# Performance work log

Hardware: AMD Instinct MI355X
Metric: run time of the kernel (lower is better)

The kernel has to match this reference:

```python
import jax, jax.numpy as jnp
import numpy as np

N_NODES = 50000
N_EDGES = 800000
IN_DIM = 128
HID = 64
HEADS = 4
OUT_DIM = 128
NEG_SLOPE = 0.2


def setup_inputs() -> dict:
    key = jax.random.key(0)
    ks = jax.random.split(key, 11)
    x = jax.random.normal(ks[0], (N_NODES, IN_DIM), dtype=jnp.float32)
    edge_index = jax.random.randint(ks[1], (2, N_EDGES), 0, N_NODES, dtype=jnp.int64)
    s1 = 1.0 / np.sqrt(IN_DIM)
    s2 = 1.0 / np.sqrt(HEADS * HID)
    W1 = jax.random.normal(ks[2], (IN_DIM, HEADS * HID), dtype=jnp.float32) * s1
    a_src1 = jax.random.normal(ks[3], (HEADS, HID), dtype=jnp.float32) * s2
    a_dst1 = jax.random.normal(ks[4], (HEADS, HID), dtype=jnp.float32) * s2
    b1 = jnp.zeros((HEADS * HID,), dtype=jnp.float32)
    W2 = jax.random.normal(ks[5], (HEADS * HID, OUT_DIM), dtype=jnp.float32) * s2
    a_src2 = jax.random.normal(ks[6], (1, OUT_DIM), dtype=jnp.float32) * 0.1
    a_dst2 = jax.random.normal(ks[7], (1, OUT_DIM), dtype=jnp.float32) * 0.1
    b2 = jnp.zeros((OUT_DIM,), dtype=jnp.float32)
    return {"x": x, "edge_index": edge_index, "W1": W1, "a_src1": a_src1,
            "a_dst1": a_dst1, "b1": b1, "W2": W2, "a_src2": a_src2,
            "a_dst2": a_dst2, "b2": b2}


def _gat_conv(x, src, dst, W, a_src, a_dst, bias, heads, out_per_head, concat):
    n = x.shape[0]
    # linear projection per head: [N, H, F]
    h = (x @ W).reshape(n, heads, out_per_head)
    # per-node attention terms: [N, H]
    alpha_src = jnp.einsum('nhf,hf->nh', h, a_src)
    alpha_dst = jnp.einsum('nhf,hf->nh', h, a_dst)
    # edge logits with LeakyReLU: [E, H]
    e = jax.nn.leaky_relu(alpha_src[src] + alpha_dst[dst], NEG_SLOPE)
    # softmax over incoming edges of each destination node
    m = jax.ops.segment_max(e, dst, num_segments=n)  # [N, H]
    m = jnp.where(jnp.isfinite(m), m, 0.0)
    e = jnp.exp(e - m[dst])
    denom = jax.ops.segment_sum(e, dst, num_segments=n)  # [N, H]
    alpha = e / (denom[dst] + 1e-16)  # [E, H]
    # weighted scatter-aggregate of source messages
    out = jax.ops.segment_sum(h[src] * alpha[:, :, None], dst, num_segments=n)  # [N, H, F]
    if concat:
        out = out.reshape(n, heads * out_per_head)
    else:
        out = out.mean(axis=1)
    return out + bias


def reference(x, edge_index, W1, a_src1, a_dst1, b1, W2, a_src2, a_dst2, b2):
    n = x.shape[0]
    # PyG GATConv adds self-loops by default
    loops = jnp.arange(n, dtype=edge_index.dtype)
    src = jnp.concatenate([edge_index[0], loops])
    dst = jnp.concatenate([edge_index[1], loops])
    # dropout layers are identity in inference
    h = _gat_conv(x, src, dst, W1, a_src1, a_dst1, b1, HEADS, HID, True)
    h = jax.nn.elu(h)
    out = _gat_conv(h, src, dst, W2, a_src2, a_dst2, b2, 1, OUT_DIM, True)
    # F.normalize(p=2, dim=1)
    norm = jnp.linalg.norm(out, axis=1, keepdims=True)
    return out / jnp.maximum(norm, 1e-12)
```

## Files before the change

kernel.cpp:

```cpp
#include <hip/hip_runtime.h>
#include <hip/hip_fp16.h>
#include <math.h>

#define N_NODES 50000
#define N_EDGES 800000
#define ET (N_EDGES + N_NODES)
#define IN_DIM 128
#define HID 64
#define HEADS 4
#define C1 (HEADS * HID)
#define OUT_DIM 128
#define NEG_SLOPE 0.2f
#define MTILES 3125
#define SCAN_B 1024
#define NSCB 49

typedef _Float16 h8 __attribute__((ext_vector_type(8)));
typedef float f4 __attribute__((ext_vector_type(4)));

__device__ __forceinline__ float leaky(float v) { return fmaxf(v, NEG_SLOPE * v); }
__device__ __forceinline__ float elu(float v) { return v > 0.0f ? v : expm1f(v); }

__device__ __forceinline__ void fma_mix8(float* acc, h8 v, float w) {
    union { h8 h; int i[4]; } u; u.h = v;
#pragma unroll
    for (int k = 0; k < 4; ++k) {
        asm("v_fma_mix_f32 %0, %1, %2, %0 op_sel:[0,0,0] op_sel_hi:[1,0,0]"
            : "+v"(acc[2 * k]) : "v"(u.i[k]), "v"(w));
        asm("v_fma_mix_f32 %0, %1, %2, %0 op_sel:[1,0,0] op_sel_hi:[1,0,0]"
            : "+v"(acc[2 * k + 1]) : "v"(u.i[k]), "v"(w));
    }
}

__global__ void prep_kernel(const float* __restrict__ W1, const float* __restrict__ W2,
                            const int* __restrict__ dst, __half* __restrict__ w1t,
                            __half* __restrict__ w2t, int* __restrict__ cnt) {
    const int tid = blockIdx.x * blockDim.x + threadIdx.x;
    const int np = gridDim.x * blockDim.x;
    for (int i = tid; i < IN_DIM * C1; i += np) {
        int k1 = i >> 8, n1 = i & 255;
        w1t[n1 * IN_DIM + k1] = __float2half(W1[i]);
        int k2 = i >> 7, n2 = i & 127;
        w2t[n2 * C1 + k2] = __float2half(W2[i]);
    }
    for (int i = tid; i < ET; i += np) {
        int d = (i < N_EDGES) ? dst[i] : i - N_EDGES;
        atomicAdd(&cnt[d], 1);
    }
}

__global__ void scan_local(const int* __restrict__ cnt, int* __restrict__ lscan,
                           int* __restrict__ bsum) {
    __shared__ int wsum[16];
    const int t = threadIdx.x, lane = t & 63, wv = t >> 6;
    int idx = blockIdx.x * SCAN_B + t;
    int v = (idx < N_NODES) ? cnt[idx] : 0;
    int sc = v;
#pragma unroll
    for (int o = 1; o < 64; o <<= 1) {
        int u = __shfl_up(sc, o);
        if (lane >= o) sc += u;
    }
    if (lane == 63) wsum[wv] = sc;
    __syncthreads();
    if (t == 0) {
        int run = 0;
#pragma unroll
        for (int w = 0; w < 16; ++w) { int s = wsum[w]; wsum[w] = run; run += s; }
        bsum[blockIdx.x] = run;
    }
    __syncthreads();
    if (idx < N_NODES) lscan[idx] = sc + wsum[wv];
}

__global__ void scan_bsum(int* __restrict__ bsum) {
    const int t = threadIdx.x;
    int v = (t < NSCB) ? bsum[t] : 0;
    int sc = v;
#pragma unroll
    for (int o = 1; o < 64; o <<= 1) {
        int u = __shfl_up(sc, o);
        if (t >= o) sc += u;
    }
    if (t < NSCB) bsum[t] = sc - v;
}

__global__ void scan_final(const int* __restrict__ cnt, const int* __restrict__ lscan,
                           const int* __restrict__ bsum, int* __restrict__ rp,
                           int* __restrict__ cursor) {
    int idx = blockIdx.x * SCAN_B + threadIdx.x;
    if (idx == 0) rp[0] = 0;
    if (idx >= N_NODES) return;
    int inc = lscan[idx] + bsum[idx >> 10];
    rp[idx + 1] = inc;
    cursor[idx] = inc - cnt[idx];
}

__global__ void scatter_kernel(const int* __restrict__ src, const int* __restrict__ dst,
                               int* __restrict__ cursor, int* __restrict__ col_src) {
    int i = blockIdx.x * blockDim.x + threadIdx.x;
    if (i >= ET) return;
    int s, d;
    if (i < N_EDGES) { s = src[i]; d = dst[i]; } else { s = d = i - N_EDGES; }
    int pos = atomicAdd(&cursor[d], 1);
    col_src[pos] = s;
}

__global__ __launch_bounds__(256) void gemm1_mfma(
        const float* __restrict__ x, const __half* __restrict__ w1t,
        const float* __restrict__ aws, const float* __restrict__ awd,
        __half* __restrict__ hpm, float* __restrict__ as1m, float* __restrict__ ad1m) {
    const int tile = blockIdx.x * 4 + (threadIdx.x >> 6);
    if (tile >= MTILES) return;
    const int lane = threadIdx.x & 63;
    const int m0 = tile * 16, lm = lane & 15, lq = lane >> 4;
    h8 afrag[4];
    const float4* xrow = (const float4*)(x + (size_t)(m0 + lm) * IN_DIM + lq * 8);
#pragma unroll
    for (int kt = 0; kt < 4; ++kt) {
        float4 a = xrow[kt * 8];
        float4 b = xrow[kt * 8 + 1];
        union { h8 v; __half2 p[4]; } u;
        u.p[0] = __floats2half2_rn(a.x, a.y);
        u.p[1] = __floats2half2_rn(a.z, a.w);
        u.p[2] = __floats2half2_rn(b.x, b.y);
        u.p[3] = __floats2half2_rn(b.z, b.w);
        afrag[kt] = u.v;
    }
    f4 acc[16];
#pragma unroll
    for (int nt = 0; nt < 16; ++nt) acc[nt] = (f4){0.f, 0.f, 0.f, 0.f};
#pragma unroll
    for (int nt = 0; nt < 16; ++nt) {
        const h8* brow = (const h8*)(w1t + (size_t)(nt * 16 + lm) * IN_DIM + lq * 8);
#pragma unroll
        for (int kt = 0; kt < 4; ++kt)
            acc[nt] = __builtin_amdgcn_mfma_f32_16x16x32_f16(afrag[kt], brow[kt * 4],
                                                             acc[nt], 0, 0, 0);
    }
    float sS[4][4] = {{0.f}}, sD[4][4] = {{0.f}};
#pragma unroll
    for (int nt = 0; nt < 16; ++nt) {
        int col = nt * 16 + lm;
        float wa = aws[col], wd = awd[col];
        int hd = nt >> 2;
        int pr = nt >> 3;
        int cip = col & 127;
#pragma unroll
        for (int r = 0; r < 4; ++r) {
            float v = acc[nt][r];
            hpm[((size_t)pr * N_NODES + (m0 + lq * 4 + r)) * 128 + cip] = __float2half(v);
            sS[hd][r] += v * wa;
            sD[hd][r] += v * wd;
        }
    }
#pragma unroll
    for (int o = 1; o < 16; o <<= 1) {
#pragma unroll
        for (int hd = 0; hd < 4; ++hd)
#pragma unroll
            for (int r = 0; r < 4; ++r) {
                sS[hd][r] += __shfl_xor(sS[hd][r], o);
                sD[hd][r] += __shfl_xor(sD[hd][r], o);
            }
    }
    if (lm == 0) {
        float2* asp = (float2*)as1m;
        float2* adp = (float2*)ad1m;
#pragma unroll
        for (int r = 0; r < 4; ++r) {
            int row = m0 + lq * 4 + r;
            asp[row]           = make_float2(sS[0][r], sS[1][r]);
            asp[N_NODES + row] = make_float2(sS[2][r], sS[3][r]);
            adp[row]           = make_float2(sD[0][r], sD[1][r]);
            adp[N_NODES + row] = make_float2(sD[2][r], sD[3][r]);
        }
    }
}

__global__ __launch_bounds__(256) void gemm2_mfma(
        const __half* __restrict__ ah, const __half* __restrict__ w2t,
        const float* __restrict__ aws, const float* __restrict__ awd,
        __half* __restrict__ h, float* __restrict__ as2, float* __restrict__ ad2) {
    const int tile = blockIdx.x * 4 + (threadIdx.x >> 6);
    if (tile >= MTILES) return;
    const int lane = threadIdx.x & 63;
    const int m0 = tile * 16, lm = lane & 15, lq = lane >> 4;
    h8 afrag[8];
    const h8* arow = (const h8*)(ah + (size_t)(m0 + lm) * C1 + lq * 8);
#pragma unroll
    for (int kt = 0; kt < 8; ++kt) afrag[kt] = arow[kt * 4];
    f4 acc[8];
#pragma unroll
    for (int nt = 0; nt < 8; ++nt) acc[nt] = (f4){0.f, 0.f, 0.f, 0.f};
#pragma unroll
    for (int nt = 0; nt < 8; ++nt) {
        const h8* brow = (const h8*)(w2t + (size_t)(nt * 16 + lm) * C1 + lq * 8);
#pragma unroll
        for (int kt = 0; kt < 8; ++kt)
            acc[nt] = __builtin_amdgcn_mfma_f32_16x16x32_f16(afrag[kt], brow[kt * 4],
                                                             acc[nt], 0, 0, 0);
    }
    float sS[4] = {0.f, 0.f, 0.f, 0.f}, sD[4] = {0.f, 0.f, 0.f, 0.f};
#pragma unroll
    for (int nt = 0; nt < 8; ++nt) {
        int col = nt * 16 + lm;
        float wa = aws[col], wd = awd[col];
#pragma unroll
        for (int r = 0; r < 4; ++r) {
            float v = acc[nt][r];
            h[(size_t)(m0 + lq * 4 + r) * OUT_DIM + col] = __float2half(v);
            sS[r] += v * wa;
            sD[r] += v * wd;
        }
    }
#pragma unroll
    for (int o = 1; o < 16; o <<= 1) {
#pragma unroll
        for (int r = 0; r < 4; ++r) {
            sS[r] += __shfl_xor(sS[r], o);
            sD[r] += __shfl_xor(sD[r], o);
        }
    }
    if (lm == 0) {
#pragma unroll
        for (int r = 0; r < 4; ++r) {
            int row = m0 + lq * 4 + r;
            as2[row] = sS[r];
            ad2[row] = sD[r];
        }
    }
}

__global__ __launch_bounds__(256) void aggregate1_fused(
        const int* __restrict__ rp, const int* __restrict__ cs,
        const __half* __restrict__ hpm, const float* __restrict__ as1m,
        const float* __restrict__ ad1m, const float* __restrict__ b1,
        __half* __restrict__ out1h) {
    __shared__ int4 stg[8][32];
    const int pair = blockIdx.x & 1, g = blockIdx.x >> 1;
    const int hw = threadIdx.x >> 5, li = threadIdx.x & 31;
    const int d = g * 8 + hw;
    const int e0 = rp[d], deg = rp[d + 1] - e0;
    const float2* asb = (const float2*)as1m + (size_t)pair * N_NODES;
    const float2 adv = ((const float2*)ad1m)[(size_t)pair * N_NODES + d];
    const char* hb = (const char*)hpm + (size_t)pair * N_NODES * 256;
    const int es = li >> 4, fl = li & 15;
    const int hip = fl >> 3;
    const int lbyte = fl * 16;
    float acc[8] = {0.f, 0.f, 0.f, 0.f, 0.f, 0.f, 0.f, 0.f};
    float ds0 = 0.f, ds1 = 0.f;
    for (int c0 = 0; c0 < deg; c0 += 32) {
        const int clen = min(32, deg - c0);
        int idx = c0 + li;
        bool valid = idx < deg;
        int s = valid ? cs[e0 + idx] : 0;
        float2 av = asb[s];
        float x0 = valid ? __expf(leaky(av.x + adv.x)) : 0.f;
        float x1 = valid ? __expf(leaky(av.y + adv.y)) : 0.f;
        stg[hw][li] = make_int4(s << 8, __float_as_int(x0), __float_as_int(x1), 0);
        ds0 += x0; ds1 += x1;
        __builtin_amdgcn_wave_barrier();
        int j = 0;
        for (; j + 8 <= clen; j += 8) {
            int4 p0 = stg[hw][j + es];
            int4 p1 = stg[hw][j + 2 + es];
            int4 p2 = stg[hw][j + 4 + es];
            int4 p3 = stg[hw][j + 6 + es];
            h8 v0 = *(const h8*)(hb + p0.x + lbyte);
            h8 v1 = *(const h8*)(hb + p1.x + lbyte);
            h8 v2 = *(const h8*)(hb + p2.x + lbyte);
            h8 v3 = *(const h8*)(hb + p3.x + lbyte);
            fma_mix8(acc, v0, __int_as_float(hip ? p0.z : p0.y));
            fma_mix8(acc, v1, __int_as_float(hip ? p1.z : p1.y));
            fma_mix8(acc, v2, __int_as_float(hip ? p2.z : p2.y));
            fma_mix8(acc, v3, __int_as_float(hip ? p3.z : p3.y));
        }
        for (; j < clen; j += 2) {
            int4 p0 = stg[hw][j + es];
            h8 v0 = *(const h8*)(hb + p0.x + lbyte);
            fma_mix8(acc, v0, __int_as_float(hip ? p0.z : p0.y));
        }
        __builtin_amdgcn_wave_barrier();
    }
#pragma unroll
    for (int f = 0; f < 8; ++f) acc[f] += __shfl_xor(acc[f], 16);
#pragma unroll
    for (int o = 16; o > 0; o >>= 1) {
        ds0 += __shfl_xor(ds0, o);
        ds1 += __shfl_xor(ds1, o);
    }
    if (es == 0) {
        float den = hip ? ds1 : ds0;
        float inv = 1.0f / (den + 1e-16f);
        float4 bA = ((const float4*)b1)[pair * 32 + fl * 2];
        float4 bB = ((const float4*)b1)[pair * 32 + fl * 2 + 1];
        h8 o;
        o[0] = (_Float16)elu(acc[0] * inv + bA.x);
        o[1] = (_Float16)elu(acc[1] * inv + bA.y);
        o[2] = (_Float16)elu(acc[2] * inv + bA.z);
        o[3] = (_Float16)elu(acc[3] * inv + bA.w);
        o[4] = (_Float16)elu(acc[4] * inv + bB.x);
        o[5] = (_Float16)elu(acc[5] * inv + bB.y);
        o[6] = (_Float16)elu(acc[6] * inv + bB.z);
        o[7] = (_Float16)elu(acc[7] * inv + bB.w);
        *(h8*)((char*)out1h + (size_t)d * 512 + pair * 256 + lbyte) = o;
    }
}

__global__ __launch_bounds__(256) void aggregate2_fused(
        const int* __restrict__ rp, const int* __restrict__ cs,
        const __half* __restrict__ h2h, const float* __restrict__ as2,
        const float* __restrict__ ad2, const float* __restrict__ b2,
        float* __restrict__ out) {
    __shared__ int2 stg[8][32];
    const int hw = threadIdx.x >> 5, li = threadIdx.x & 31;
    const int d = blockIdx.x * 8 + hw;
    const int e0 = rp[d], deg = rp[d + 1] - e0;
    const float adv = ad2[d];
    const int q = li >> 4, lo = li & 15;
    const int lbyte = lo * 16;
    const char* hbase = (const char*)h2h;
    float acc[8] = {0.f, 0.f, 0.f, 0.f, 0.f, 0.f, 0.f, 0.f};
    float dsum = 0.f;
    for (int c0 = 0; c0 < deg; c0 += 32) {
        const int clen = min(32, deg - c0);
        int idx = c0 + li;
        bool valid = idx < deg;
        int s = valid ? cs[e0 + idx] : 0;
        float x = valid ? __expf(leaky(as2[s] + adv)) : 0.f;
        stg[hw][li] = make_int2(valid ? (s << 8) : 0, __float_as_int(x));
        dsum += x;
        __builtin_amdgcn_wave_barrier();
        int j = 0;
        for (; j + 8 <= clen; j += 8) {
            int2 p0 = stg[hw][j + q];
            int2 p1 = stg[hw][j + 2 + q];
            int2 p2 = stg[hw][j + 4 + q];
            int2 p3 = stg[hw][j + 6 + q];
            h8 v0 = *(const h8*)(hbase + p0.x + lbyte);
            h8 v1 = *(const h8*)(hbase + p1.x + lbyte);
            h8 v2 = *(const h8*)(hbase + p2.x + lbyte);
            h8 v3 = *(const h8*)(hbase + p3.x + lbyte);
            fma_mix8(acc, v0, __int_as_float(p0.y));
            fma_mix8(acc, v1, __int_as_float(p1.y));
            fma_mix8(acc, v2, __int_as_float(p2.y));
            fma_mix8(acc, v3, __int_as_float(p3.y));
        }
        for (; j < clen; j += 2) {
            int2 p0 = stg[hw][j + q];
            h8 v0 = *(const h8*)(hbase + p0.x + lbyte);
            fma_mix8(acc, v0, __int_as_float(p0.y));
        }
        __builtin_amdgcn_wave_barrier();
    }
#pragma unroll
    for (int f = 0; f < 8; ++f) acc[f] += __shfl_xor(acc[f], 16);
#pragma unroll
    for (int o = 16; o > 0; o >>= 1) dsum += __shfl_xor(dsum, o);
    if (q == 0) {
        float inv = 1.0f / (dsum + 1e-16f);
        float4 bA = ((const float4*)b2)[lo * 2];
        float4 bB = ((const float4*)b2)[lo * 2 + 1];
        float v0 = acc[0] * inv + bA.x, v1 = acc[1] * inv + bA.y;
        float v2 = acc[2] * inv + bA.z, v3 = acc[3] * inv + bA.w;
        float v4 = acc[4] * inv + bB.x, v5 = acc[5] * inv + bB.y;
        float v6 = acc[6] * inv + bB.z, v7 = acc[7] * inv + bB.w;
        float ss = v0 * v0 + v1 * v1 + v2 * v2 + v3 * v3 +
                   v4 * v4 + v5 * v5 + v6 * v6 + v7 * v7;
#pragma unroll
        for (int o = 1; o < 16; o <<= 1) ss += __shfl_xor(ss, o);
        float sc = 1.0f / fmaxf(sqrtf(ss), 1e-12f);
        float4* orow = (float4*)((char*)out + (size_t)d * 512 + lo * 32);
        orow[0] = make_float4(v0 * sc, v1 * sc, v2 * sc, v3 * sc);
        orow[1] = make_float4(v4 * sc, v5 * sc, v6 * sc, v7 * sc);
    }
}

extern "C" void kernel_launch(void* const* d_in, const int* in_sizes, int n_in,
                              void* d_out, int out_size, void* d_ws, size_t ws_size,
                              hipStream_t stream) {
    const float* x     = (const float*)d_in[0];
    const int*   edge  = (const int*)d_in[1];
    const int*   src   = edge;
    const int*   dst   = edge + N_EDGES;
    const float* W1    = (const float*)d_in[2];
    const float* aw_s1 = (const float*)d_in[3];
    const float* aw_d1 = (const float*)d_in[4];
    const float* b1    = (const float*)d_in[5];
    const float* W2    = (const float*)d_in[6];
    const float* aw_s2 = (const float*)d_in[7];
    const float* aw_d2 = (const float*)d_in[8];
    const float* b2    = (const float*)d_in[9];
    float* out = (float*)d_out;

    char* ws = (char*)d_ws;
    size_t off = 0;
    auto alloc = [&](size_t bytes) {
        void* p = ws + off;
        off += (bytes + 255) & ~(size_t)255;
        return p;
    };
    int*    col_src = (int*)alloc((size_t)ET * 4);
    int*    rp     = (int*)alloc((size_t)(N_NODES + 1) * 4);
    int*    cursor = (int*)alloc((size_t)N_NODES * 4);
    int*    cnt    = (int*)alloc((size_t)N_NODES * 4);
    int*    lscan  = (int*)alloc((size_t)NSCB * SCAN_B * 4);
    int*    bsum   = (int*)alloc((size_t)NSCB * 4);
    float*  as1    = (float*)alloc((size_t)N_NODES * HEADS * 4);
    float*  ad1    = (float*)alloc((size_t)N_NODES * HEADS * 4);
    float*  as2    = (float*)alloc((size_t)N_NODES * 4);
    float*  ad2    = (float*)alloc((size_t)N_NODES * 4);
    __half* w1t    = (__half*)alloc((size_t)IN_DIM * C1 * 2);
    __half* w2t    = (__half*)alloc((size_t)C1 * OUT_DIM * 2);
    __half* hpm    = (__half*)alloc((size_t)N_NODES * C1 * 2);
    __half* out1h  = (__half*)alloc((size_t)N_NODES * C1 * 2);
    __half* h2h    = hpm;
    (void)off;

    hipMemsetAsync(cnt, 0, (size_t)N_NODES * 4, stream);

    const int egrid = (ET + 255) / 256;

    prep_kernel<<<1024, 256, 0, stream>>>(W1, W2, dst, w1t, w2t, cnt);
    scan_local<<<NSCB, SCAN_B, 0, stream>>>(cnt, lscan, bsum);
    scan_bsum<<<1, 64, 0, stream>>>(bsum);
    scan_final<<<NSCB, SCAN_B, 0, stream>>>(cnt, lscan, bsum, rp, cursor);
    scatter_kernel<<<egrid, 256, 0, stream>>>(src, dst, cursor, col_src);

    gemm1_mfma<<<(MTILES + 3) / 4, 256, 0, stream>>>(x, w1t, aw_s1, aw_d1, hpm, as1, ad1);
    aggregate1_fused<<<(N_NODES / 8) * 2, 256, 0, stream>>>(rp, col_src, hpm, as1, ad1, b1, out1h);

    gemm2_mfma<<<(MTILES + 3) / 4, 256, 0, stream>>>(out1h, w2t, aw_s2, aw_d2, h2h, as2, ad2);
    aggregate2_fused<<<N_NODES / 8, 256, 0, stream>>>(rp, col_src, h2h, as2, ad2, b2, out);
}
```

Measured before the change: 349.0 us.

## Split layer-2 features into column halves for aggregation, normalize in separate pass

gemm2 now writes its fp16 output in a column-split layout: two contiguous 64-column planes, each 128 bytes per node. aggregate2 runs twice as many blocks, and each block gathers only one half-plane, which matches how layer 1 is aggregated. The aim is a smaller gather footprint per block and more parallelism. Because each block now sees only half a row, the L2 norm is built by atomically adding partial sums into a new zeroed buffer. A separate norm_kernel then rescales the output, adding a launch and an extra read-write pass over the output.

```diff
diff --git a/kernel.cpp b/kernel.cpp
--- a/kernel.cpp
+++ b/kernel.cpp
@@ -181,7 +181,7 @@
 __global__ __launch_bounds__(256) void gemm2_mfma(
         const __half* __restrict__ ah, const __half* __restrict__ w2t,
         const float* __restrict__ aws, const float* __restrict__ awd,
-        __half* __restrict__ h, float* __restrict__ as2, float* __restrict__ ad2) {
+        __half* __restrict__ h2c, float* __restrict__ as2, float* __restrict__ ad2) {
     const int tile = blockIdx.x * 4 + (threadIdx.x >> 6);
     if (tile >= MTILES) return;
     const int lane = threadIdx.x & 63;
@@ -206,10 +206,12 @@
     for (int nt = 0; nt < 8; ++nt) {
         int col = nt * 16 + lm;
         float wa = aws[col], wd = awd[col];
+        int half = nt >> 2;
+        int cih = col & 63;
 #pragma unroll
         for (int r = 0; r < 4; ++r) {
             float v = acc[nt][r];
-            h[(size_t)(m0 + lq * 4 + r) * OUT_DIM + col] = __float2half(v);
+            h2c[((size_t)half * N_NODES + (m0 + lq * 4 + r)) * 64 + cih] = __float2half(v);
             sS[r] += v * wa;
             sD[r] += v * wd;
         }
@@ -308,19 +310,20 @@
     }
 }
 
-__global__ __launch_bounds__(256) void aggregate2_fused(
+__global__ __launch_bounds__(256) void aggregate2_half(
         const int* __restrict__ rp, const int* __restrict__ cs,
-        const __half* __restrict__ h2h, const float* __restrict__ as2,
+        const __half* __restrict__ h2c, const float* __restrict__ as2,
         const float* __restrict__ ad2, const float* __restrict__ b2,
-        float* __restrict__ out) {
+        float* __restrict__ out, float* __restrict__ ss) {
     __shared__ int2 stg[8][32];
+    const int half = blockIdx.x & 1, g = blockIdx.x >> 1;
     const int hw = threadIdx.x >> 5, li = threadIdx.x & 31;
-    const int d = blockIdx.x * 8 + hw;
+    const int d = g * 8 + hw;
     const int e0 = rp[d], deg = rp[d + 1] - e0;
     const float adv = ad2[d];
-    const int q = li >> 4, lo = li & 15;
-    const int lbyte = lo * 16;
-    const char* hbase = (const char*)h2h;
+    const char* hb = (const char*)h2c + (size_t)half * N_NODES * 128;
+    const int es = li >> 3, fl = li & 7;
+    const int lbyte = fl * 16;
     float acc[8] = {0.f, 0.f, 0.f, 0.f, 0.f, 0.f, 0.f, 0.f};
     float dsum = 0.f;
     for (int c0 = 0; c0 < deg; c0 += 32) {
@@ -328,53 +331,67 @@
         int idx = c0 + li;
         bool valid = idx < deg;
         int s = valid ? cs[e0 + idx] : 0;
-        float x = valid ? __expf(leaky(as2[s] + adv)) : 0.f;
-        stg[hw][li] = make_int2(valid ? (s << 8) : 0, __float_as_int(x));
-        dsum += x;
+        float xv = valid ? __expf(leaky(as2[s] + adv)) : 0.f;
+        stg[hw][li] = make_int2(s << 7, __float_as_int(xv));
+        dsum += xv;
         __builtin_amdgcn_wave_barrier();
         int j = 0;
-        for (; j + 8 <= clen; j += 8) {
-            int2 p0 = stg[hw][j + q];
-            int2 p1 = stg[hw][j + 2 + q];
-            int2 p2 = stg[hw][j + 4 + q];
-            int2 p3 = stg[hw][j + 6 + q];
-            h8 v0 = *(const h8*)(hbase + p0.x + lbyte);
-            h8 v1 = *(const h8*)(hbase + p1.x + lbyte);
-            h8 v2 = *(const h8*)(hbase + p2.x + lbyte);
-            h8 v3 = *(const h8*)(hbase + p3.x + lbyte);
+        for (; j + 16 <= clen; j += 16) {
+            int2 p0 = stg[hw][j + es];
+            int2 p1 = stg[hw][j + 4 + es];
+            int2 p2 = stg[hw][j + 8 + es];
+            int2 p3 = stg[hw][j + 12 + es];
+            h8 v0 = *(const h8*)(hb + p0.x + lbyte);
+            h8 v1 = *(const h8*)(hb + p1.x + lbyte);
+            h8 v2 = *(const h8*)(hb + p2.x + lbyte);
+            h8 v3 = *(const h8*)(hb + p3.x + lbyte);
             fma_mix8(acc, v0, __int_as_float(p0.y));
             fma_mix8(acc, v1, __int_as_float(p1.y));
             fma_mix8(acc, v2, __int_as_float(p2.y));
             fma_mix8(acc, v3, __int_as_float(p3.y));
         }
-        for (; j < clen; j += 2) {
-            int2 p0 = stg[hw][j + q];
-            h8 v0 = *(const h8*)(hbase + p0.x + lbyte);
+        for (; j < clen; j += 4) {
+            int2 p0 = stg[hw][j + es];
+            h8 v0 = *(const h8*)(hb + p0.x + lbyte);
             fma_mix8(acc, v0, __int_as_float(p0.y));
         }
         __builtin_amdgcn_wave_barrier();
     }
 #pragma unroll
-    for (int f = 0; f < 8; ++f) acc[f] += __shfl_xor(acc[f], 16);
+    for (int f = 0; f < 8; ++f) {
+        acc[f] += __shfl_xor(acc[f], 8);
+        acc[f] += __shfl_xor(acc[f], 16);
+    }
 #pragma unroll
     for (int o = 16; o > 0; o >>= 1) dsum += __shfl_xor(dsum, o);
-    if (q == 0) {
+    if (es == 0) {
         float inv = 1.0f / (dsum + 1e-16f);
-        float4 bA = ((const float4*)b2)[lo * 2];
-        float4 bB = ((const float4*)b2)[lo * 2 + 1];
+        float4 bA = ((const float4*)b2)[half * 16 + fl * 2];
+        float4 bB = ((const float4*)b2)[half * 16 + fl * 2 + 1];
         float v0 = acc[0] * inv + bA.x, v1 = acc[1] * inv + bA.y;
         float v2 = acc[2] * inv + bA.z, v3 = acc[3] * inv + bA.w;
         float v4 = acc[4] * inv + bB.x, v5 = acc[5] * inv + bB.y;
         float v6 = acc[6] * inv + bB.z, v7 = acc[7] * inv + bB.w;
-        float ss = v0 * v0 + v1 * v1 + v2 * v2 + v3 * v3 +
+        float sp = v0 * v0 + v1 * v1 + v2 * v2 + v3 * v3 +
                    v4 * v4 + v5 * v5 + v6 * v6 + v7 * v7;
 #pragma unroll
-        for (int o = 1; o < 16; o <<= 1) ss += __shfl_xor(ss, o);
-        float sc = 1.0f / fmaxf(sqrtf(ss), 1e-12f);
-        float4* orow = (float4*)((char*)out + (size_t)d * 512 + lo * 32);
-        orow[0] = make_float4(v0 * sc, v1 * sc, v2 * sc, v3 * sc);
-        orow[1] = make_float4(v4 * sc, v5 * sc, v6 * sc, v7 * sc);
-    }
+        for (int o = 1; o < 8; o <<= 1) sp += __shfl_xor(sp, o);
+        if (fl == 0) atomicAdd(&ss[d], sp);
+        float4* orow = (float4*)(out + (size_t)d * OUT_DIM + half * 64 + fl * 8);
+        orow[0] = make_float4(v0, v1, v2, v3);
+        orow[1] = make_float4(v4, v5, v6, v7);
+    }
+}
+
+__global__ __launch_bounds__(256) void norm_kernel(const float* __restrict__ ss,
+                                                   float* __restrict__ out) {
+    int idx = blockIdx.x * 256 + threadIdx.x;
+    int row = idx >> 5, c = idx & 31;
+    if (row >= N_NODES) return;
+    float sc = 1.0f / fmaxf(sqrtf(ss[row]), 1e-12f);
+    float4* p = (float4*)out + (size_t)row * 32 + c;
+    float4 v = *p;
+    *p = make_float4(v.x * sc, v.y * sc, v.z * sc, v.w * sc);
 }
 
 extern "C" void kernel_launch(void* const* d_in, const int* in_sizes, int n_in,
@@ -405,6 +422,7 @@
     int*    rp     = (int*)alloc((size_t)(N_NODES + 1) * 4);
     int*    cursor = (int*)alloc((size_t)N_NODES * 4);
     int*    cnt    = (int*)alloc((size_t)N_NODES * 4);
+    float*  ss     = (float*)alloc((size_t)N_NODES * 4);
     int*    lscan  = (int*)alloc((size_t)NSCB * SCAN_B * 4);
     int*    bsum   = (int*)alloc((size_t)NSCB * 4);
     float*  as1    = (float*)alloc((size_t)N_NODES * HEADS * 4);
@@ -415,10 +433,11 @@
     __half* w2t    = (__half*)alloc((size_t)C1 * OUT_DIM * 2);
     __half* hpm    = (__half*)alloc((size_t)N_NODES * C1 * 2);
     __half* out1h  = (__half*)alloc((size_t)N_NODES * C1 * 2);
-    __half* h2h    = hpm;
+    __half* h2c    = hpm;
     (void)off;
 
-    hipMemsetAsync(cnt, 0, (size_t)N_NODES * 4, stream);
+    const size_t cnt_rounded = ((size_t)N_NODES * 4 + 255) & ~(size_t)255;
+    hipMemsetAsync(cnt, 0, cnt_rounded + (size_t)N_NODES * 4, stream);
 
     const int egrid = (ET + 255) / 256;
 
@@ -431,6 +450,7 @@
     gemm1_mfma<<<(MTILES + 3) / 4, 256, 0, stream>>>(x, w1t, aw_s1, aw_d1, hpm, as1, ad1);
     aggregate1_fused<<<(N_NODES / 8) * 2, 256, 0, stream>>>(rp, col_src, hpm, as1, ad1, b1, out1h);
 
-    gemm2_mfma<<<(MTILES + 3) / 4, 256, 0, stream>>>(out1h, w2t, aw_s2, aw_d2, h2h, as2, ad2);
-    aggregate2_fused<<<N_NODES / 8, 256, 0, stream>>>(rp, col_src, h2h, as2, ad2, b2, out);
-}
+    gemm2_mfma<<<(MTILES + 3) / 4, 256, 0, stream>>>(out1h, w2t, aw_s2, aw_d2, h2c, as2, ad2);
+    aggregate2_half<<<(N_NODES / 8) * 2, 256, 0, stream>>>(rp, col_src, h2c, as2, ad2, b2, out, ss);
+    norm_kernel<<<(N_NODES * 32 + 255) / 256, 256, 0, stream>>>(ss, out);
+}
```

Result: slower. 364.0 us (+4.3%).

## Fuse edge scatter into gemm1 and store CSR source indices as 16-bit

Applied to the files above, without the earlier changes.

Merges the edge scatter kernel into the first GEMM launch by interleaving block roles: one in five blocks does an MFMA tile, the other four do scatter. This removes a kernel launch and lets the atomic scatter overlap with GEMM work. Column source indices are stored as uint16 to halve CSR index traffic, which depends on node ids staying below 65536. Both aggregation kernels also gain a 16-edge unrolled loop to keep more gathers in flight, at the cost of more register pressure.

```diff
diff --git a/kernel.cpp b/kernel.cpp
--- a/kernel.cpp
+++ b/kernel.cpp
@@ -14,9 +14,12 @@
 #define MTILES 3125
 #define SCAN_B 1024
 #define NSCB 49
+#define SCB 3328
+#define FUSED_GRID 4160
 
 typedef _Float16 h8 __attribute__((ext_vector_type(8)));
 typedef float f4 __attribute__((ext_vector_type(4)));
+typedef unsigned short u16;
 
 __device__ __forceinline__ float leaky(float v) { return fmaxf(v, NEG_SLOPE * v); }
 __device__ __forceinline__ float elu(float v) { return v > 0.0f ? v : expm1f(v); }
@@ -96,21 +99,25 @@
     cursor[idx] = inc - cnt[idx];
 }
 
-__global__ void scatter_kernel(const int* __restrict__ src, const int* __restrict__ dst,
-                               int* __restrict__ cursor, int* __restrict__ col_src) {
-    int i = blockIdx.x * blockDim.x + threadIdx.x;
-    if (i >= ET) return;
-    int s, d;
-    if (i < N_EDGES) { s = src[i]; d = dst[i]; } else { s = d = i - N_EDGES; }
-    int pos = atomicAdd(&cursor[d], 1);
-    col_src[pos] = s;
-}
-
-__global__ __launch_bounds__(256) void gemm1_mfma(
+__global__ __launch_bounds__(256) void gemm1_scatter(
         const float* __restrict__ x, const __half* __restrict__ w1t,
         const float* __restrict__ aws, const float* __restrict__ awd,
-        __half* __restrict__ hpm, float* __restrict__ as1m, float* __restrict__ ad1m) {
-    const int tile = blockIdx.x * 4 + (threadIdx.x >> 6);
+        __half* __restrict__ hpm, float* __restrict__ as1m, float* __restrict__ ad1m,
+        const int* __restrict__ src, const int* __restrict__ dst,
+        int* __restrict__ cursor, u16* __restrict__ cs16) {
+    const int q5 = blockIdx.x / 5, r5 = blockIdx.x % 5;
+    if (r5 != 0) {
+        int si = q5 * 4 + (r5 - 1);
+        int i = si * 256 + threadIdx.x;
+        if (i < ET) {
+            int s, d;
+            if (i < N_EDGES) { s = src[i]; d = dst[i]; } else { s = d = i - N_EDGES; }
+            int pos = atomicAdd(&cursor[d], 1);
+            cs16[pos] = (u16)s;
+        }
+        return;
+    }
+    const int tile = q5 * 4 + (threadIdx.x >> 6);
     if (tile >= MTILES) return;
     const int lane = threadIdx.x & 63;
     const int m0 = tile * 16, lm = lane & 15, lq = lane >> 4;
@@ -233,7 +240,7 @@
 }
 
 __global__ __launch_bounds__(256) void aggregate1_fused(
-        const int* __restrict__ rp, const int* __restrict__ cs,
+        const int* __restrict__ rp, const u16* __restrict__ cs16,
         const __half* __restrict__ hpm, const float* __restrict__ as1m,
         const float* __restrict__ ad1m, const float* __restrict__ b1,
         __half* __restrict__ out1h) {
@@ -254,7 +261,7 @@
         const int clen = min(32, deg - c0);
         int idx = c0 + li;
         bool valid = idx < deg;
-        int s = valid ? cs[e0 + idx] : 0;
+        int s = valid ? (int)cs16[e0 + idx] : 0;
         float2 av = asb[s];
         float x0 = valid ? __expf(leaky(av.x + adv.x)) : 0.f;
         float x1 = valid ? __expf(leaky(av.y + adv.y)) : 0.f;
@@ -262,6 +269,32 @@
         ds0 += x0; ds1 += x1;
         __builtin_amdgcn_wave_barrier();
         int j = 0;
+        for (; j + 16 <= clen; j += 16) {
+            int4 p0 = stg[hw][j + es];
+            int4 p1 = stg[hw][j + 2 + es];
+            int4 p2 = stg[hw][j + 4 + es];
+            int4 p3 = stg[hw][j + 6 + es];
+            int4 p4 = stg[hw][j + 8 + es];
+            int4 p5 = stg[hw][j + 10 + es];
+            int4 p6 = stg[hw][j + 12 + es];
+            int4 p7 = stg[hw][j + 14 + es];
+            h8 v0 = *(const h8*)(hb + p0.x + lbyte);
+            h8 v1 = *(const h8*)(hb + p1.x + lbyte);
+            h8 v2 = *(const h8*)(hb + p2.x + lbyte);
+            h8 v3 = *(const h8*)(hb + p3.x + lbyte);
+            h8 v4 = *(const h8*)(hb + p4.x + lbyte);
+            h8 v5 = *(const h8*)(hb + p5.x + lbyte);
+            h8 v6 = *(const h8*)(hb + p6.x + lbyte);
+            h8 v7 = *(const h8*)(hb + p7.x + lbyte);
+            fma_mix8(acc, v0, __int_as_float(hip ? p0.z : p0.y));
+            fma_mix8(acc, v1, __int_as_float(hip ? p1.z : p1.y));
+            fma_mix8(acc, v2, __int_as_float(hip ? p2.z : p2.y));
+            fma_mix8(acc, v3, __int_as_float(hip ? p3.z : p3.y));
+            fma_mix8(acc, v4, __int_as_float(hip ? p4.z : p4.y));
+            fma_mix8(acc, v5, __int_as_float(hip ? p5.z : p5.y));
+            fma_mix8(acc, v6, __int_as_float(hip ? p6.z : p6.y));
+            fma_mix8(acc, v7, __int_as_float(hip ? p7.z : p7.y));
+        }
         for (; j + 8 <= clen; j += 8) {
             int4 p0 = stg[hw][j + es];
             int4 p1 = stg[hw][j + 2 + es];
@@ -309,7 +342,7 @@
 }
 
 __global__ __launch_bounds__(256) void aggregate2_fused(
-        const int* __restrict__ rp, const int* __restrict__ cs,
+        const int* __restrict__ rp, const u16* __restrict__ cs16,
         const __half* __restrict__ h2h, const float* __restrict__ as2,
         const float* __restrict__ ad2, const float* __restrict__ b2,
         float* __restrict__ out) {
@@ -327,12 +360,38 @@
         const int clen = min(32, deg - c0);
         int idx = c0 + li;
         bool valid = idx < deg;
-        int s = valid ? cs[e0 + idx] : 0;
-        float x = valid ? __expf(leaky(as2[s] + adv)) : 0.f;
-        stg[hw][li] = make_int2(valid ? (s << 8) : 0, __float_as_int(x));
-        dsum += x;
+        int s = valid ? (int)cs16[e0 + idx] : 0;
+        float xv = valid ? __expf(leaky(as2[s] + adv)) : 0.f;
+        stg[hw][li] = make_int2(s << 8, __float_as_int(xv));
+        dsum += xv;
         __builtin_amdgcn_wave_barrier();
         int j = 0;
+        for (; j + 16 <= clen; j += 16) {
+            int2 p0 = stg[hw][j + q];
+            int2 p1 = stg[hw][j + 2 + q];
+            int2 p2 = stg[hw][j + 4 + q];
+            int2 p3 = stg[hw][j + 6 + q];
+            int2 p4 = stg[hw][j + 8 + q];
+            int2 p5 = stg[hw][j + 10 + q];
+            int2 p6 = stg[hw][j + 12 + q];
+            int2 p7 = stg[hw][j + 14 + q];
+            h8 v0 = *(const h8*)(hbase + p0.x + lbyte);
+            h8 v1 = *(const h8*)(hbase + p1.x + lbyte);
+            h8 v2 = *(const h8*)(hbase + p2.x + lbyte);
+            h8 v3 = *(const h8*)(hbase + p3.x + lbyte);
+            h8 v4 = *(const h8*)(hbase + p4.x + lbyte);
+            h8 v5 = *(const h8*)(hbase + p5.x + lbyte);
+            h8 v6 = *(const h8*)(hbase + p6.x + lbyte);
+            h8 v7 = *(const h8*)(hbase + p7.x + lbyte);
+            fma_mix8(acc, v0, __int_as_float(p0.y));
+            fma_mix8(acc, v1, __int_as_float(p1.y));
+            fma_mix8(acc, v2, __int_as_float(p2.y));
+            fma_mix8(acc, v3, __int_as_float(p3.y));
+            fma_mix8(acc, v4, __int_as_float(p4.y));
+            fma_mix8(acc, v5, __int_as_float(p5.y));
+            fma_mix8(acc, v6, __int_as_float(p6.y));
+            fma_mix8(acc, v7, __int_as_float(p7.y));
+        }
         for (; j + 8 <= clen; j += 8) {
             int2 p0 = stg[hw][j + q];
             int2 p1 = stg[hw][j + 2 + q];
@@ -401,7 +460,7 @@
         off += (bytes + 255) & ~(size_t)255;
         return p;
     };
-    int*    col_src = (int*)alloc((size_t)ET * 4);
+    u16*    cs16   = (u16*)alloc((size_t)ET * 2);
     int*    rp     = (int*)alloc((size_t)(N_NODES + 1) * 4);
     int*    cursor = (int*)alloc((size_t)N_NODES * 4);
     int*    cnt    = (int*)alloc((size_t)N_NODES * 4);
@@ -420,17 +479,16 @@
 
     hipMemsetAsync(cnt, 0, (size_t)N_NODES * 4, stream);
 
-    const int egrid = (ET + 255) / 256;
-
     prep_kernel<<<1024, 256, 0, stream>>>(W1, W2, dst, w1t, w2t, cnt);
     scan_local<<<NSCB, SCAN_B, 0, stream>>>(cnt, lscan, bsum);
     scan_bsum<<<1, 64, 0, stream>>>(bsum);
     scan_final<<<NSCB, SCAN_B, 0, stream>>>(cnt, lscan, bsum, rp, cursor);
-    scatter_kernel<<<egrid, 256, 0, stream>>>(src, dst, cursor, col_src);
-
-    gemm1_mfma<<<(MTILES + 3) / 4, 256, 0, stream>>>(x, w1t, aw_s1, aw_d1, hpm, as1, ad1);
-    aggregate1_fused<<<(N_NODES / 8) * 2, 256, 0, stream>>>(rp, col_src, hpm, as1, ad1, b1, out1h);
+
+    gemm1_scatter<<<FUSED_GRID, 256, 0, stream>>>(x, w1t, aw_s1, aw_d1, hpm, as1, ad1,
+                                                  src, dst, cursor, cs16);
+
+    aggregate1_fused<<<(N_NODES / 8) * 2, 256, 0, stream>>>(rp, cs16, hpm, as1, ad1, b1, out1h);
 
     gemm2_mfma<<<(MTILES + 3) / 4, 256, 0, stream>>>(out1h, w2t, aw_s2, aw_d2, h2h, as2, ad2);
-    aggregate2_fused<<<N_NODES / 8, 256, 0, stream>>>(rp, col_src, h2h, as2, ad2, b2, out);
-}
+    aggregate2_fused<<<N_NODES / 8, 256, 0, stream>>>(rp, cs16, h2h, as2, ad2, b2, out);
+}
```

New measurement: 332.1 us. 1.05x faster.

## Record atomic ranks during counting and store CSR columns as 16-bit

Applied to the files above, without the earlier changes.

The degree-counting pass now saves each edge's atomic return value as a 16-bit rank, so the scatter pass computes final CSR positions without a second round of atomics and the cursor array goes away. Self-loops are appended analytically at the end of each row instead of being counted. Column indices are stored as uint16, which halves index traffic in both aggregation kernels. This relies on N_NODES < 65536 and per-node degree fitting in 16 bits, and it changes the within-row order of edges.

```diff
diff --git a/kernel.cpp b/kernel.cpp
--- a/kernel.cpp
+++ b/kernel.cpp
@@ -17,6 +17,7 @@
 
 typedef _Float16 h8 __attribute__((ext_vector_type(8)));
 typedef float f4 __attribute__((ext_vector_type(4)));
+typedef unsigned short u16;
 
 __device__ __forceinline__ float leaky(float v) { return fmaxf(v, NEG_SLOPE * v); }
 __device__ __forceinline__ float elu(float v) { return v > 0.0f ? v : expm1f(v); }
@@ -34,7 +35,8 @@
 
 __global__ void prep_kernel(const float* __restrict__ W1, const float* __restrict__ W2,
                             const int* __restrict__ dst, __half* __restrict__ w1t,
-                            __half* __restrict__ w2t, int* __restrict__ cnt) {
+                            __half* __restrict__ w2t, int* __restrict__ cnt,
+                            u16* __restrict__ rank16) {
     const int tid = blockIdx.x * blockDim.x + threadIdx.x;
     const int np = gridDim.x * blockDim.x;
     for (int i = tid; i < IN_DIM * C1; i += np) {
@@ -43,9 +45,13 @@
         int k2 = i >> 7, n2 = i & 127;
         w2t[n2 * C1 + k2] = __float2half(W2[i]);
     }
-    for (int i = tid; i < ET; i += np) {
-        int d = (i < N_EDGES) ? dst[i] : i - N_EDGES;
-        atomicAdd(&cnt[d], 1);
+    if (tid < N_EDGES / 4) {
+        int4 d4 = ((const int4*)dst)[tid];
+        int r0 = atomicAdd(&cnt[d4.x], 1);
+        int r1 = atomicAdd(&cnt[d4.y], 1);
+        int r2 = atomicAdd(&cnt[d4.z], 1);
+        int r3 = atomicAdd(&cnt[d4.w], 1);
+        ((ushort4*)rank16)[tid] = make_ushort4((u16)r0, (u16)r1, (u16)r2, (u16)r3);
     }
 }
 
@@ -54,7 +60,7 @@
     __shared__ int wsum[16];
     const int t = threadIdx.x, lane = t & 63, wv = t >> 6;
     int idx = blockIdx.x * SCAN_B + t;
-    int v = (idx < N_NODES) ? cnt[idx] : 0;
+    int v = (idx < N_NODES) ? cnt[idx] + 1 : 0;
     int sc = v;
 #pragma unroll
     for (int o = 1; o < 64; o <<= 1) {
@@ -85,25 +91,34 @@
     if (t < NSCB) bsum[t] = sc - v;
 }
 
-__global__ void scan_final(const int* __restrict__ cnt, const int* __restrict__ lscan,
-                           const int* __restrict__ bsum, int* __restrict__ rp,
-                           int* __restrict__ cursor) {
+__global__ void scan_final(const int* __restrict__ lscan, const int* __restrict__ bsum,
+                           int* __restrict__ rp) {
     int idx = blockIdx.x * SCAN_B + threadIdx.x;
     if (idx == 0) rp[0] = 0;
     if (idx >= N_NODES) return;
-    int inc = lscan[idx] + bsum[idx >> 10];
-    rp[idx + 1] = inc;
-    cursor[idx] = inc - cnt[idx];
-}
-
-__global__ void scatter_kernel(const int* __restrict__ src, const int* __restrict__ dst,
-                               int* __restrict__ cursor, int* __restrict__ col_src) {
-    int i = blockIdx.x * blockDim.x + threadIdx.x;
-    if (i >= ET) return;
-    int s, d;
-    if (i < N_EDGES) { s = src[i]; d = dst[i]; } else { s = d = i - N_EDGES; }
-    int pos = atomicAdd(&cursor[d], 1);
-    col_src[pos] = s;
+    rp[idx + 1] = lscan[idx] + bsum[idx >> 10];
+}
+
+__global__ void scatter_plain(const int* __restrict__ src, const int* __restrict__ dst,
+                              const u16* __restrict__ rank16, const int* __restrict__ rp,
+                              u16* __restrict__ cs16) {
+    const int tid = blockIdx.x * blockDim.x + threadIdx.x;
+    if (tid < N_EDGES / 4) {
+        int4 s4 = ((const int4*)src)[tid];
+        int4 d4 = ((const int4*)dst)[tid];
+        ushort4 r4 = ((const ushort4*)rank16)[tid];
+        int p0 = rp[d4.x] + (int)r4.x;
+        int p1 = rp[d4.y] + (int)r4.y;
+        int p2 = rp[d4.z] + (int)r4.z;
+        int p3 = rp[d4.w] + (int)r4.w;
+        cs16[p0] = (u16)s4.x;
+        cs16[p1] = (u16)s4.y;
+        cs16[p2] = (u16)s4.z;
+        cs16[p3] = (u16)s4.w;
+    } else {
+        int d = tid - N_EDGES / 4;
+        if (d < N_NODES) cs16[rp[d + 1] - 1] = (u16)d;
+    }
 }
 
 __global__ __launch_bounds__(256) void gemm1_mfma(
@@ -233,7 +248,7 @@
 }
 
 __global__ __launch_bounds__(256) void aggregate1_fused(
-        const int* __restrict__ rp, const int* __restrict__ cs,
+        const int* __restrict__ rp, const u16* __restrict__ cs16,
         const __half* __restrict__ hpm, const float* __restrict__ as1m,
         const float* __restrict__ ad1m, const float* __restrict__ b1,
         __half* __restrict__ out1h) {
@@ -254,7 +269,7 @@
         const int clen = min(32, deg - c0);
         int idx = c0 + li;
         bool valid = idx < deg;
-        int s = valid ? cs[e0 + idx] : 0;
+        int s = valid ? (int)cs16[e0 + idx] : 0;
         float2 av = asb[s];
         float x0 = valid ? __expf(leaky(av.x + adv.x)) : 0.f;
         float x1 = valid ? __expf(leaky(av.y + adv.y)) : 0.f;
@@ -309,7 +324,7 @@
 }
 
 __global__ __launch_bounds__(256) void aggregate2_fused(
-        const int* __restrict__ rp, const int* __restrict__ cs,
+        const int* __restrict__ rp, const u16* __restrict__ cs16,
         const __half* __restrict__ h2h, const float* __restrict__ as2,
         const float* __restrict__ ad2, const float* __restrict__ b2,
         float* __restrict__ out) {
@@ -327,10 +342,10 @@
         const int clen = min(32, deg - c0);
         int idx = c0 + li;
         bool valid = idx < deg;
-        int s = valid ? cs[e0 + idx] : 0;
-        float x = valid ? __expf(leaky(as2[s] + adv)) : 0.f;
-        stg[hw][li] = make_int2(valid ? (s << 8) : 0, __float_as_int(x));
-        dsum += x;
+        int s = valid ? (int)cs16[e0 + idx] : 0;
+        float xv = valid ? __expf(leaky(as2[s] + adv)) : 0.f;
+        stg[hw][li] = make_int2(s << 8, __float_as_int(xv));
+        dsum += xv;
         __builtin_amdgcn_wave_barrier();
         int j = 0;
         for (; j + 8 <= clen; j += 8) {
@@ -401,9 +416,9 @@
         off += (bytes + 255) & ~(size_t)255;
         return p;
     };
-    int*    col_src = (int*)alloc((size_t)ET * 4);
+    u16*    cs16   = (u16*)alloc((size_t)ET * 2);
+    u16*    rank16 = (u16*)alloc((size_t)N_EDGES * 2);
     int*    rp     = (int*)alloc((size_t)(N_NODES + 1) * 4);
-    int*    cursor = (int*)alloc((size_t)N_NODES * 4);
     int*    cnt    = (int*)alloc((size_t)N_NODES * 4);
     int*    lscan  = (int*)alloc((size_t)NSCB * SCAN_B * 4);
     int*    bsum   = (int*)alloc((size_t)NSCB * 4);
@@ -420,17 +435,16 @@
 
     hipMemsetAsync(cnt, 0, (size_t)N_NODES * 4, stream);
 
-    const int egrid = (ET + 255) / 256;
-
-    prep_kernel<<<1024, 256, 0, stream>>>(W1, W2, dst, w1t, w2t, cnt);
+    prep_kernel<<<1024, 256, 0, stream>>>(W1, W2, dst, w1t, w2t, cnt, rank16);
     scan_local<<<NSCB, SCAN_B, 0, stream>>>(cnt, lscan, bsum);
     scan_bsum<<<1, 64, 0, stream>>>(bsum);
-    scan_final<<<NSCB, SCAN_B, 0, stream>>>(cnt, lscan, bsum, rp, cursor);
-    scatter_kernel<<<egrid, 256, 0, stream>>>(src, dst, cursor, col_src);
+    scan_final<<<NSCB, SCAN_B, 0, stream>>>(lscan, bsum, rp);
+    scatter_plain<<<(N_EDGES / 4 + N_NODES + 255) / 256, 256, 0, stream>>>(
+        src, dst, rank16, rp, cs16);
 
     gemm1_mfma<<<(MTILES + 3) / 4, 256, 0, stream>>>(x, w1t, aw_s1, aw_d1, hpm, as1, ad1);
-    aggregate1_fused<<<(N_NODES / 8) * 2, 256, 0, stream>>>(rp, col_src, hpm, as1, ad1, b1, out1h);
+    aggregate1_fused<<<(N_NODES / 8) * 2, 256, 0, stream>>>(rp, cs16, hpm, as1, ad1, b1, out1h);
 
     gemm2_mfma<<<(MTILES + 3) / 4, 256, 0, stream>>>(out1h, w2t, aw_s2, aw_d2, h2h, as2, ad2);
-    aggregate2_fused<<<N_NODES / 8, 256, 0, stream>>>(rp, col_src, h2h, as2, ad2, b2, out);
-}
+    aggregate2_fused<<<N_NODES / 8, 256, 0, stream>>>(rp, cs16, h2h, as2, ad2, b2, out);
+}
```

Result: faster. 310.7 us (-11.0%).
